# Kernel tuning notes

Measured on AMD Instinct MI355X. Metric: run time of the kernel, lower is better.

Reference implementation:

```python
import jax, jax.numpy as jnp
import numpy as np
import math

B, N, K, H = 2, 2048, 1024, 16
S = K // H  # head dim = 64


def apply_rope(t):
    # t: [b, h, N, s] -> rotary position embedding (rotate-half convention)
    s = t.shape[-1]
    pos = jnp.arange(t.shape[2], dtype=jnp.float32)
    inv_freq = 1.0 / (10000.0 ** (jnp.arange(0, s, 2, dtype=jnp.float32) / s))
    ang = pos[:, None] * inv_freq[None, :]               # [N, s/2]
    cos = jnp.concatenate([jnp.cos(ang), jnp.cos(ang)], axis=-1)  # [N, s]
    sin = jnp.concatenate([jnp.sin(ang), jnp.sin(ang)], axis=-1)
    t1, t2 = t[..., : s // 2], t[..., s // 2:]
    rot = jnp.concatenate([-t2, t1], axis=-1)
    return t * cos + rot * sin


def setup_inputs() -> dict:
    key = jax.random.key(0)
    ks = jax.random.split(key, 6)
    sc = 1.0 / math.sqrt(K)
    x = jax.random.normal(ks[0], (B, N, K), dtype=jnp.float32)
    Wq = jax.random.normal(ks[1], (K, K), dtype=jnp.float32) * sc
    Wk = jax.random.normal(ks[2], (K, K), dtype=jnp.float32) * sc
    Wv = jax.random.normal(ks[3], (K, K), dtype=jnp.float32) * sc
    Wu = jax.random.normal(ks[4], (K, K), dtype=jnp.float32) * sc
    bu = jax.random.normal(ks[5], (K,), dtype=jnp.float32) * 0.01
    mask = jnp.tril(jnp.ones((N, N), dtype=jnp.int32))  # causal
    return {"x": x, "Wq": Wq, "Wk": Wk, "Wv": Wv, "Wu": Wu, "bu": bu, "mask": mask}


def reference(x, Wq, Wk, Wv, Wu, bu, mask):
    b, n, k = x.shape
    h, s = H, S
    # torch Linear: y = x @ W.T
    def proj(W):
        return (x @ W.T).reshape(b, n, h, s).transpose(0, 2, 1, 3)  # [b,h,n,s]
    Q = apply_rope(proj(Wq))
    Kh = apply_rope(proj(Wk))
    V = proj(Wv)
    scores = jnp.einsum('bhqs,bhks->bhqk', Q, Kh) / math.sqrt(s)
    scores = jnp.where(mask[None, None, :, :] == 0, -jnp.inf, scores)
    attn = jax.nn.softmax(scores, axis=-1)
    out = jnp.einsum('bhqk,bhks->bhqs', attn, V)           # [b,h,n,s]
    out = out.transpose(0, 2, 1, 3).reshape(b, n, k)
    return out @ Wu.T + bu
```

## Files before the change

### kernel.cpp

```cpp
#include <hip/hip_runtime.h>
#include <hip/hip_bf16.h>

#define Bq 2
#define Nq 2048
#define Kq 1024
#define Hq 16
#define Sq 64
#define Mq (Bq * Nq)

typedef __attribute__((ext_vector_type(4))) float f32x4;
typedef __attribute__((ext_vector_type(8))) short bf16x8;

__device__ unsigned short g_xb[(size_t)Mq * Kq];
__device__ unsigned short g_Wqb[Kq * Kq];
__device__ unsigned short g_Wkb[Kq * Kq];
__device__ unsigned short g_Wvb[Kq * Kq];
__device__ unsigned short g_Wub[Kq * Kq];
__device__ unsigned short g_Qb[(size_t)Bq * Hq * Nq * Sq];
__device__ unsigned short g_Kb[(size_t)Bq * Hq * Nq * Sq];
__device__ unsigned short g_Vb[(size_t)Bq * Hq * Nq * Sq];
__device__ unsigned short g_Vt[(size_t)Bq * Hq * Sq * Nq];
__device__ unsigned short g_Ao[(size_t)Mq * Kq];

__device__ __forceinline__ unsigned short f2bf(float f) {
    union { float f; unsigned int i; } u; u.f = f;
    unsigned int r = u.i + 0x7FFF + ((u.i >> 16) & 1);
    return (unsigned short)(r >> 16);
}
__device__ __forceinline__ float bf2f(unsigned short u) {
    union { unsigned int i; float f; } v; v.i = ((unsigned int)u) << 16;
    return v.f;
}
__device__ __forceinline__ void async16(const unsigned short* g, unsigned short* l) {
    __builtin_amdgcn_global_load_lds(
        (const __attribute__((address_space(1))) void*)g,
        (__attribute__((address_space(3))) void*)l, 16, 0, 0);
}

__global__ __launch_bounds__(256) void convert_all_kernel(
    const float* __restrict__ x,  const float* __restrict__ wq,
    const float* __restrict__ wk, const float* __restrict__ wv,
    const float* __restrict__ wu)
{
    int i = blockIdx.x * 256 + threadIdx.x;
    const float* src; unsigned short* dst; int off;
    if (i < 1048576) { src = x; dst = g_xb; off = i; }
    else {
        int j = i - 1048576;
        int which = j >> 18;
        off = j & 262143;
        src = (which == 0) ? wq : (which == 1) ? wk : (which == 2) ? wv : wu;
        dst = (which == 0) ? g_Wqb : (which == 1) ? g_Wkb : (which == 2) ? g_Wvb : g_Wub;
    }
    float4 v = ((const float4*)src)[off];
    ushort4 o;
    o.x = f2bf(v.x); o.y = f2bf(v.y); o.z = f2bf(v.z); o.w = f2bf(v.w);
    ((ushort4*)dst)[off] = o;
}

__global__ __launch_bounds__(256) void qkv_gemm_kernel()
{
    __shared__ __align__(16) unsigned short As[128][64];
    __shared__ __align__(16) unsigned short Bs[128][64];

    const int n0 = blockIdx.x * 128;
    const int m0 = blockIdx.y * 128;
    const int which = n0 >> 10;
    const unsigned short* A  = g_xb;
    const unsigned short* Bm = (which == 0) ? g_Wqb : (which == 1) ? g_Wkb : g_Wvb;
    unsigned short* dst      = (which == 0) ? g_Qb : (which == 1) ? g_Kb : g_Vb;
    const int nb = n0 & 1023;

    const int tid = threadIdx.x;
    const int w = tid >> 6, l = tid & 63;
    const int lane16 = l & 15, quad = l >> 4;
    const int wm = (w >> 1) * 64, wn = (w & 1) * 64;

    const int sr = l >> 3;
    const int sc = ((l & 7) ^ sr) * 8;
    const int rsw = (lane16 & 7);

    f32x4 acc[4][4];
#pragma unroll
    for (int mi = 0; mi < 4; ++mi)
#pragma unroll
        for (int ni = 0; ni < 4; ++ni) acc[mi][ni] = (f32x4){0.f, 0.f, 0.f, 0.f};

    for (int kt = 0; kt < Kq; kt += 64) {
        __syncthreads();
#pragma unroll
        for (int c = 0; c < 4; ++c) {
            async16(A  + (size_t)(m0 + 32 * w + 8 * c + sr) * Kq + kt + sc, &As[32 * w + 8 * c][0]);
            async16(Bm + (size_t)(nb + 32 * w + 8 * c + sr) * Kq + kt + sc, &Bs[32 * w + 8 * c][0]);
        }
        __syncthreads();
#pragma unroll
        for (int ks = 0; ks < 2; ++ks) {
            bf16x8 af[4], bfr[4];
#pragma unroll
            for (int mi = 0; mi < 4; ++mi)
                af[mi]  = *(const bf16x8*)&As[wm + mi * 16 + lane16][((ks * 4 + quad) ^ rsw) * 8];
#pragma unroll
            for (int ni = 0; ni < 4; ++ni)
                bfr[ni] = *(const bf16x8*)&Bs[wn + ni * 16 + lane16][((ks * 4 + quad) ^ rsw) * 8];
#pragma unroll
            for (int mi = 0; mi < 4; ++mi)
#pragma unroll
                for (int ni = 0; ni < 4; ++ni)
                    acc[mi][ni] = __builtin_amdgcn_mfma_f32_16x16x32_bf16(af[mi], bfr[ni], acc[mi][ni], 0, 0, 0);
        }
    }

#pragma unroll
    for (int mi = 0; mi < 4; ++mi)
#pragma unroll
        for (int ni = 0; ni < 4; ++ni)
#pragma unroll
            for (int r = 0; r < 4; ++r) {
                int m = m0 + wm + mi * 16 + quad * 4 + r;
                int n = n0 + wn + ni * 16 + lane16;
                unsigned short v = f2bf(acc[mi][ni][r]);
                int b = m >> 11, nn = m & 2047;
                int o = n & 1023, h = o >> 6, s = o & 63;
                dst[(((size_t)b * Hq + h) * Nq + nn) * Sq + s] = v;
            }
}

__global__ __launch_bounds__(256) void rope_kernel()
{
    unsigned short* buf = (blockIdx.y == 0) ? g_Qb : g_Kb;
    const int idx = blockIdx.x * 256 + threadIdx.x;
    const int i  = idx & 31;
    const int n  = (idx >> 5) & (Nq - 1);
    const int bh = idx >> 16;
    const size_t base = ((size_t)bh * Nq + n) * Sq + i;

    float t1 = bf2f(buf[base]);
    float t2 = bf2f(buf[base + 32]);
    float inv_freq = powf(10000.0f, -(float)i / 32.0f);
    float ang = (float)n * inv_freq;
    float sn, cs;
    sincosf(ang, &sn, &cs);
    buf[base]      = f2bf(t1 * cs - t2 * sn);
    buf[base + 32] = f2bf(t2 * cs + t1 * sn);
}

__global__ __launch_bounds__(256) void vtrans_kernel()
{
    __shared__ unsigned short T[64][72];
    const int n0 = blockIdx.x * 64;
    const int bh = blockIdx.y;
    const unsigned short* src = g_Vb + (size_t)bh * Nq * Sq;
    unsigned short* dst       = g_Vt + (size_t)bh * Sq * Nq;
    const int tid = threadIdx.x;
    const int r = tid >> 3, c8 = (tid & 7) * 8;

    uint4 a0 = *(const uint4*)(src + (size_t)(n0 + r) * Sq + c8);
    uint4 a1 = *(const uint4*)(src + (size_t)(n0 + r + 32) * Sq + c8);
    *(uint4*)&T[r][c8] = a0;
    *(uint4*)&T[r + 32][c8] = a1;
    __syncthreads();

    union { ushort4 u4[2]; unsigned short u[8]; } p0, p1;
#pragma unroll
    for (int j = 0; j < 8; ++j) { p0.u[j] = T[c8 + j][r]; p1.u[j] = T[c8 + j][r + 32]; }
    *(uint4*)(dst + (size_t)r * Nq + n0 + c8)        = *(uint4*)&p0;
    *(uint4*)(dst + (size_t)(r + 32) * Nq + n0 + c8) = *(uint4*)&p1;
}

__global__ __launch_bounds__(256) void attn_kernel()
{
    const int bh = blockIdx.x;
    const int qt = 31 - (int)blockIdx.y;
    const int q0 = qt * 64;
    const unsigned short* Qp = g_Qb + (size_t)bh * Nq * Sq;
    const unsigned short* Kp = g_Kb + (size_t)bh * Nq * Sq;
    const unsigned short* Vp = g_Vt + (size_t)bh * Sq * Nq;

    __shared__ __align__(16) unsigned short Ks[2][64][64];
    __shared__ __align__(16) unsigned short Vs[2][64][64];
    __shared__ __align__(16) unsigned short On[16][72];
    __shared__ __align__(16) unsigned short Ps[64][72];

    const int tid = threadIdx.x;
    const int w = tid >> 6, l = tid & 63;
    const int lane16 = l & 15, quad = l >> 4;
    const int sr = l >> 3;
    const int sc = ((l & 7) ^ sr) * 8;
    const int rsw = (lane16 & 7);

    for (int i = tid; i < 16 * 72; i += 256)
        ((unsigned short*)On)[i] = (i < 64) ? 0x3F80 : 0;

    bf16x8 aq0 = *(const bf16x8*)(Qp + (size_t)(q0 + 16 * w + lane16) * Sq + quad * 8);
    bf16x8 aq1 = *(const bf16x8*)(Qp + (size_t)(q0 + 16 * w + lane16) * Sq + quad * 8 + 32);

    f32x4 Oacc[4];
    f32x4 Oext = (f32x4){0.f, 0.f, 0.f, 0.f};
#pragma unroll
    for (int ds = 0; ds < 4; ++ds) Oacc[ds] = (f32x4){0.f, 0.f, 0.f, 0.f};

    const float C1 = 0.18033688f;
    const float C2 = 11.54156036f;

    async16(Kp + (size_t)(16 * w + sr) * Sq + sc,     &Ks[0][16 * w][0]);
    async16(Kp + (size_t)(16 * w + 8 + sr) * Sq + sc, &Ks[0][16 * w + 8][0]);
    async16(Vp + (size_t)(16 * w + sr) * Nq + sc,     &Vs[0][16 * w][0]);
    async16(Vp + (size_t)(16 * w + 8 + sr) * Nq + sc, &Vs[0][16 * w + 8][0]);
    __syncthreads();

    int cur = 0;
    for (int kb = 0; kb <= qt; ++kb) {
        if (kb < qt) {
            int kn = (kb + 1) * 64;
            int nb2 = cur ^ 1;
            async16(Kp + (size_t)(kn + 16 * w + sr) * Sq + sc,     &Ks[nb2][16 * w][0]);
            async16(Kp + (size_t)(kn + 16 * w + 8 + sr) * Sq + sc, &Ks[nb2][16 * w + 8][0]);
            async16(Vp + (size_t)(16 * w + sr) * Nq + kn + sc,     &Vs[nb2][16 * w][0]);
            async16(Vp + (size_t)(16 * w + 8 + sr) * Nq + kn + sc, &Vs[nb2][16 * w + 8][0]);
        }

        f32x4 S[4];
#pragma unroll
        for (int kc = 0; kc < 4; ++kc) S[kc] = (f32x4){0.f, 0.f, 0.f, 0.f};
#pragma unroll
        for (int kc = 0; kc < 4; ++kc) {
            const unsigned short* krow = &Ks[cur][kc * 16 + lane16][0];
            bf16x8 bk0 = *(const bf16x8*)&krow[(quad ^ rsw) * 8];
            bf16x8 bk1 = *(const bf16x8*)&krow[((4 + quad) ^ rsw) * 8];
            S[kc] = __builtin_amdgcn_mfma_f32_16x16x32_bf16(aq0, bk0, S[kc], 0, 0, 0);
            S[kc] = __builtin_amdgcn_mfma_f32_16x16x32_bf16(aq1, bk1, S[kc], 0, 0, 0);
        }

        const int qbase = q0 + 16 * w + quad * 4;
        if (kb == qt) {
#pragma unroll
            for (int kc = 0; kc < 4; ++kc) {
                int kpos = kb * 64 + kc * 16 + lane16;
#pragma unroll
                for (int r = 0; r < 4; ++r)
                    S[kc][r] = (kpos <= qbase + r) ? exp2f(fmaf(S[kc][r], C1, -C2)) : 0.0f;
            }
        } else {
#pragma unroll
            for (int kc = 0; kc < 4; ++kc)
#pragma unroll
                for (int r = 0; r < 4; ++r)
                    S[kc][r] = exp2f(fmaf(S[kc][r], C1, -C2));
        }

#pragma unroll
        for (int kc = 0; kc < 4; ++kc)
#pragma unroll
            for (int r = 0; r < 4; ++r)
                Ps[16 * w + quad * 4 + r][kc * 16 + lane16] =
                    (unsigned short)(__float_as_uint(S[kc][r]) >> 16);

#pragma unroll
        for (int kk = 0; kk < 2; ++kk) {
            bf16x8 pa = *(const bf16x8*)&Ps[16 * w + lane16][kk * 32 + quad * 8];
            bf16x8 be = *(const bf16x8*)&On[lane16][kk * 32 + quad * 8];
#pragma unroll
            for (int ds = 0; ds < 4; ++ds) {
                bf16x8 vb = *(const bf16x8*)&Vs[cur][ds * 16 + lane16][((kk * 4 + quad) ^ rsw) * 8];
                Oacc[ds] = __builtin_amdgcn_mfma_f32_16x16x32_bf16(pa, vb, Oacc[ds], 0, 0, 0);
            }
            Oext = __builtin_amdgcn_mfma_f32_16x16x32_bf16(pa, be, Oext, 0, 0, 0);
        }

        __syncthreads();
        cur ^= 1;
    }

    const int b = bh >> 4, h = bh & 15;
    float inv[4];
#pragma unroll
    for (int r = 0; r < 4; ++r) {
        float lr = __shfl(Oext[r], quad * 16, 64);
        inv[r] = 1.0f / lr;
    }
#pragma unroll
    for (int ds = 0; ds < 4; ++ds)
#pragma unroll
        for (int r = 0; r < 4; ++r) {
            int nn = q0 + 16 * w + quad * 4 + r;
            g_Ao[((size_t)b * Nq + nn) * Kq + h * Sq + ds * 16 + lane16] =
                f2bf(Oacc[ds][r] * inv[r]);
        }
}

__global__ __launch_bounds__(256) void out_gemm_kernel(
    const float* __restrict__ bu, float* __restrict__ out)
{
    __shared__ __align__(16) unsigned short As[128][64];
    __shared__ __align__(16) unsigned short Bs[128][64];

    const int n0 = blockIdx.x * 128;
    const int m0 = blockIdx.y * 128;

    const int tid = threadIdx.x;
    const int w = tid >> 6, l = tid & 63;
    const int lane16 = l & 15, quad = l >> 4;
    const int wm = (w >> 1) * 64, wn = (w & 1) * 64;
    const int sr = l >> 3;
    const int sc = ((l & 7) ^ sr) * 8;
    const int rsw = (lane16 & 7);

    f32x4 acc[4][4];
#pragma unroll
    for (int mi = 0; mi < 4; ++mi)
#pragma unroll
        for (int ni = 0; ni < 4; ++ni) acc[mi][ni] = (f32x4){0.f, 0.f, 0.f, 0.f};

    for (int kt = 0; kt < Kq; kt += 64) {
        __syncthreads();
#pragma unroll
        for (int c = 0; c < 4; ++c) {
            async16(g_Ao  + (size_t)(m0 + 32 * w + 8 * c + sr) * Kq + kt + sc, &As[32 * w + 8 * c][0]);
            async16(g_Wub + (size_t)(n0 + 32 * w + 8 * c + sr) * Kq + kt + sc, &Bs[32 * w + 8 * c][0]);
        }
        __syncthreads();
#pragma unroll
        for (int ks = 0; ks < 2; ++ks) {
            bf16x8 af[4], bfr[4];
#pragma unroll
            for (int mi = 0; mi < 4; ++mi)
                af[mi]  = *(const bf16x8*)&As[wm + mi * 16 + lane16][((ks * 4 + quad) ^ rsw) * 8];
#pragma unroll
            for (int ni = 0; ni < 4; ++ni)
                bfr[ni] = *(const bf16x8*)&Bs[wn + ni * 16 + lane16][((ks * 4 + quad) ^ rsw) * 8];
#pragma unroll
            for (int mi = 0; mi < 4; ++mi)
#pragma unroll
                for (int ni = 0; ni < 4; ++ni)
                    acc[mi][ni] = __builtin_amdgcn_mfma_f32_16x16x32_bf16(af[mi], bfr[ni], acc[mi][ni], 0, 0, 0);
        }
    }

#pragma unroll
    for (int mi = 0; mi < 4; ++mi)
#pragma unroll
        for (int ni = 0; ni < 4; ++ni)
#pragma unroll
            for (int r = 0; r < 4; ++r) {
                int m = m0 + wm + mi * 16 + quad * 4 + r;
                int n = n0 + wn + ni * 16 + lane16;
                out[(size_t)m * Kq + n] = acc[mi][ni][r] + bu[n];
            }
}

extern "C" void kernel_launch(void* const* d_in, const int* in_sizes, int n_in,
                              void* d_out, int out_size, void* d_ws, size_t ws_size,
                              hipStream_t stream)
{
    const float* x  = (const float*)d_in[0];
    const float* Wq = (const float*)d_in[1];
    const float* Wk = (const float*)d_in[2];
    const float* Wv = (const float*)d_in[3];
    const float* Wu = (const float*)d_in[4];
    const float* bu = (const float*)d_in[5];
    float* out = (float*)d_out;

    convert_all_kernel<<<8192, 256, 0, stream>>>(x, Wq, Wk, Wv, Wu);
    qkv_gemm_kernel<<<dim3(24, 32), 256, 0, stream>>>();
    vtrans_kernel<<<dim3(32, 32), 256, 0, stream>>>();
    rope_kernel<<<dim3((Bq * Hq * Nq * 32) / 256, 2), 256, 0, stream>>>();
    attn_kernel<<<dim3(32, 32), 256, 0, stream>>>();
    out_gemm_kernel<<<dim3(8, 32), 256, 0, stream>>>(bu, out);
}
```

Baseline: 228.3 us.

## Double-buffer GEMM LDS tiles, merge rope and V-transpose, use fast trig

Both GEMM kernels now keep two shared-memory buffers and issue the async loads for the next K tile before computing the current one. This replaces two barriers per iteration with one and overlaps global-to-LDS traffic with MFMA work. The rope and V-transpose kernels are merged into one launch, and the rope angle uses exp2f plus __sinf/__cosf instead of powf and sincosf. The costs are double the LDS per block, which may lower occupancy, and lower trig accuracy at large angles, which could matter for positions near 2047. The merged launch also wastes many idle blocks in its V-transpose row, since only 1024 of its 8192 blocks do work.

```diff
diff --git a/kernel.cpp b/kernel.cpp
--- a/kernel.cpp
+++ b/kernel.cpp
@@ -60,8 +60,8 @@
 
 __global__ __launch_bounds__(256) void qkv_gemm_kernel()
 {
-    __shared__ __align__(16) unsigned short As[128][64];
-    __shared__ __align__(16) unsigned short Bs[128][64];
+    __shared__ __align__(16) unsigned short As[2][128][64];
+    __shared__ __align__(16) unsigned short Bs[2][128][64];
 
     const int n0 = blockIdx.x * 128;
     const int m0 = blockIdx.y * 128;
@@ -86,29 +86,40 @@
 #pragma unroll
         for (int ni = 0; ni < 4; ++ni) acc[mi][ni] = (f32x4){0.f, 0.f, 0.f, 0.f};
 
+#pragma unroll
+    for (int c = 0; c < 4; ++c) {
+        async16(A  + (size_t)(m0 + 32 * w + 8 * c + sr) * Kq + sc, &As[0][32 * w + 8 * c][0]);
+        async16(Bm + (size_t)(nb + 32 * w + 8 * c + sr) * Kq + sc, &Bs[0][32 * w + 8 * c][0]);
+    }
+    __syncthreads();
+
+    int cur = 0;
     for (int kt = 0; kt < Kq; kt += 64) {
-        __syncthreads();
-#pragma unroll
-        for (int c = 0; c < 4; ++c) {
-            async16(A  + (size_t)(m0 + 32 * w + 8 * c + sr) * Kq + kt + sc, &As[32 * w + 8 * c][0]);
-            async16(Bm + (size_t)(nb + 32 * w + 8 * c + sr) * Kq + kt + sc, &Bs[32 * w + 8 * c][0]);
-        }
-        __syncthreads();
+        if (kt + 64 < Kq) {
+            int nxt = cur ^ 1;
+#pragma unroll
+            for (int c = 0; c < 4; ++c) {
+                async16(A  + (size_t)(m0 + 32 * w + 8 * c + sr) * Kq + kt + 64 + sc, &As[nxt][32 * w + 8 * c][0]);
+                async16(Bm + (size_t)(nb + 32 * w + 8 * c + sr) * Kq + kt + 64 + sc, &Bs[nxt][32 * w + 8 * c][0]);
+            }
+        }
 #pragma unroll
         for (int ks = 0; ks < 2; ++ks) {
             bf16x8 af[4], bfr[4];
 #pragma unroll
             for (int mi = 0; mi < 4; ++mi)
-                af[mi]  = *(const bf16x8*)&As[wm + mi * 16 + lane16][((ks * 4 + quad) ^ rsw) * 8];
+                af[mi]  = *(const bf16x8*)&As[cur][wm + mi * 16 + lane16][((ks * 4 + quad) ^ rsw) * 8];
 #pragma unroll
             for (int ni = 0; ni < 4; ++ni)
-                bfr[ni] = *(const bf16x8*)&Bs[wn + ni * 16 + lane16][((ks * 4 + quad) ^ rsw) * 8];
+                bfr[ni] = *(const bf16x8*)&Bs[cur][wn + ni * 16 + lane16][((ks * 4 + quad) ^ rsw) * 8];
 #pragma unroll
             for (int mi = 0; mi < 4; ++mi)
 #pragma unroll
                 for (int ni = 0; ni < 4; ++ni)
                     acc[mi][ni] = __builtin_amdgcn_mfma_f32_16x16x32_bf16(af[mi], bfr[ni], acc[mi][ni], 0, 0, 0);
         }
+        __syncthreads();
+        cur ^= 1;
     }
 
 #pragma unroll
@@ -126,46 +137,46 @@
             }
 }
 
-__global__ __launch_bounds__(256) void rope_kernel()
-{
-    unsigned short* buf = (blockIdx.y == 0) ? g_Qb : g_Kb;
-    const int idx = blockIdx.x * 256 + threadIdx.x;
-    const int i  = idx & 31;
-    const int n  = (idx >> 5) & (Nq - 1);
-    const int bh = idx >> 16;
-    const size_t base = ((size_t)bh * Nq + n) * Sq + i;
-
-    float t1 = bf2f(buf[base]);
-    float t2 = bf2f(buf[base + 32]);
-    float inv_freq = powf(10000.0f, -(float)i / 32.0f);
-    float ang = (float)n * inv_freq;
-    float sn, cs;
-    sincosf(ang, &sn, &cs);
-    buf[base]      = f2bf(t1 * cs - t2 * sn);
-    buf[base + 32] = f2bf(t2 * cs + t1 * sn);
-}
-
-__global__ __launch_bounds__(256) void vtrans_kernel()
+__global__ __launch_bounds__(256) void rope_vtrans_kernel()
 {
     __shared__ unsigned short T[64][72];
-    const int n0 = blockIdx.x * 64;
-    const int bh = blockIdx.y;
-    const unsigned short* src = g_Vb + (size_t)bh * Nq * Sq;
-    unsigned short* dst       = g_Vt + (size_t)bh * Sq * Nq;
-    const int tid = threadIdx.x;
-    const int r = tid >> 3, c8 = (tid & 7) * 8;
-
-    uint4 a0 = *(const uint4*)(src + (size_t)(n0 + r) * Sq + c8);
-    uint4 a1 = *(const uint4*)(src + (size_t)(n0 + r + 32) * Sq + c8);
-    *(uint4*)&T[r][c8] = a0;
-    *(uint4*)&T[r + 32][c8] = a1;
-    __syncthreads();
-
-    union { ushort4 u4[2]; unsigned short u[8]; } p0, p1;
-#pragma unroll
-    for (int j = 0; j < 8; ++j) { p0.u[j] = T[c8 + j][r]; p1.u[j] = T[c8 + j][r + 32]; }
-    *(uint4*)(dst + (size_t)r * Nq + n0 + c8)        = *(uint4*)&p0;
-    *(uint4*)(dst + (size_t)(r + 32) * Nq + n0 + c8) = *(uint4*)&p1;
+
+    if (blockIdx.y < 2) {
+        unsigned short* buf = (blockIdx.y == 0) ? g_Qb : g_Kb;
+        const int idx = blockIdx.x * 256 + threadIdx.x;
+        const int i  = idx & 31;
+        const int n  = (idx >> 5) & (Nq - 1);
+        const int bh = idx >> 16;
+        const size_t base = ((size_t)bh * Nq + n) * Sq + i;
+
+        float t1 = bf2f(buf[base]);
+        float t2 = bf2f(buf[base + 32]);
+        float inv_freq = exp2f((float)i * -0.41524101f);
+        float ang = (float)n * inv_freq;
+        float sn = __sinf(ang), cs = __cosf(ang);
+        buf[base]      = f2bf(t1 * cs - t2 * sn);
+        buf[base + 32] = f2bf(t2 * cs + t1 * sn);
+    } else {
+        if (blockIdx.x >= 1024) return;
+        const int n0 = (blockIdx.x & 31) * 64;
+        const int bh = blockIdx.x >> 5;
+        const unsigned short* src = g_Vb + (size_t)bh * Nq * Sq;
+        unsigned short* dst       = g_Vt + (size_t)bh * Sq * Nq;
+        const int tid = threadIdx.x;
+        const int r = tid >> 3, c8 = (tid & 7) * 8;
+
+        uint4 a0 = *(const uint4*)(src + (size_t)(n0 + r) * Sq + c8);
+        uint4 a1 = *(const uint4*)(src + (size_t)(n0 + r + 32) * Sq + c8);
+        *(uint4*)&T[r][c8] = a0;
+        *(uint4*)&T[r + 32][c8] = a1;
+        __syncthreads();
+
+        union { ushort4 u4[2]; unsigned short u[8]; } p0, p1;
+#pragma unroll
+        for (int j = 0; j < 8; ++j) { p0.u[j] = T[c8 + j][r]; p1.u[j] = T[c8 + j][r + 32]; }
+        *(uint4*)(dst + (size_t)r * Nq + n0 + c8)        = *(uint4*)&p0;
+        *(uint4*)(dst + (size_t)(r + 32) * Nq + n0 + c8) = *(uint4*)&p1;
+    }
 }
 
 __global__ __launch_bounds__(256) void attn_kernel()
@@ -292,8 +303,8 @@
 __global__ __launch_bounds__(256) void out_gemm_kernel(
     const float* __restrict__ bu, float* __restrict__ out)
 {
-    __shared__ __align__(16) unsigned short As[128][64];
-    __shared__ __align__(16) unsigned short Bs[128][64];
+    __shared__ __align__(16) unsigned short As[2][128][64];
+    __shared__ __align__(16) unsigned short Bs[2][128][64];
 
     const int n0 = blockIdx.x * 128;
     const int m0 = blockIdx.y * 128;
@@ -312,29 +323,40 @@
 #pragma unroll
         for (int ni = 0; ni < 4; ++ni) acc[mi][ni] = (f32x4){0.f, 0.f, 0.f, 0.f};
 
+#pragma unroll
+    for (int c = 0; c < 4; ++c) {
+        async16(g_Ao  + (size_t)(m0 + 32 * w + 8 * c + sr) * Kq + sc, &As[0][32 * w + 8 * c][0]);
+        async16(g_Wub + (size_t)(n0 + 32 * w + 8 * c + sr) * Kq + sc, &Bs[0][32 * w + 8 * c][0]);
+    }
+    __syncthreads();
+
+    int cur = 0;
     for (int kt = 0; kt < Kq; kt += 64) {
-        __syncthreads();
-#pragma unroll
-        for (int c = 0; c < 4; ++c) {
-            async16(g_Ao  + (size_t)(m0 + 32 * w + 8 * c + sr) * Kq + kt + sc, &As[32 * w + 8 * c][0]);
-            async16(g_Wub + (size_t)(n0 + 32 * w + 8 * c + sr) * Kq + kt + sc, &Bs[32 * w + 8 * c][0]);
-        }
-        __syncthreads();
+        if (kt + 64 < Kq) {
+            int nxt = cur ^ 1;
+#pragma unroll
+            for (int c = 0; c < 4; ++c) {
+                async16(g_Ao  + (size_t)(m0 + 32 * w + 8 * c + sr) * Kq + kt + 64 + sc, &As[nxt][32 * w + 8 * c][0]);
+                async16(g_Wub + (size_t)(n0 + 32 * w + 8 * c + sr) * Kq + kt + 64 + sc, &Bs[nxt][32 * w + 8 * c][0]);
+            }
+        }
 #pragma unroll
         for (int ks = 0; ks < 2; ++ks) {
             bf16x8 af[4], bfr[4];
 #pragma unroll
             for (int mi = 0; mi < 4; ++mi)
-                af[mi]  = *(const bf16x8*)&As[wm + mi * 16 + lane16][((ks * 4 + quad) ^ rsw) * 8];
+                af[mi]  = *(const bf16x8*)&As[cur][wm + mi * 16 + lane16][((ks * 4 + quad) ^ rsw) * 8];
 #pragma unroll
             for (int ni = 0; ni < 4; ++ni)
-                bfr[ni] = *(const bf16x8*)&Bs[wn + ni * 16 + lane16][((ks * 4 + quad) ^ rsw) * 8];
+                bfr[ni] = *(const bf16x8*)&Bs[cur][wn + ni * 16 + lane16][((ks * 4 + quad) ^ rsw) * 8];
 #pragma unroll
             for (int mi = 0; mi < 4; ++mi)
 #pragma unroll
                 for (int ni = 0; ni < 4; ++ni)
                     acc[mi][ni] = __builtin_amdgcn_mfma_f32_16x16x32_bf16(af[mi], bfr[ni], acc[mi][ni], 0, 0, 0);
         }
+        __syncthreads();
+        cur ^= 1;
     }
 
 #pragma unroll
@@ -363,8 +385,7 @@
 
     convert_all_kernel<<<8192, 256, 0, stream>>>(x, Wq, Wk, Wv, Wu);
     qkv_gemm_kernel<<<dim3(24, 32), 256, 0, stream>>>();
-    vtrans_kernel<<<dim3(32, 32), 256, 0, stream>>>();
-    rope_kernel<<<dim3((Bq * Hq * Nq * 32) / 256, 2), 256, 0, stream>>>();
+    rope_vtrans_kernel<<<dim3(8192, 3), 256, 0, stream>>>();
     attn_kernel<<<dim3(32, 32), 256, 0, stream>>>();
     out_gemm_kernel<<<dim3(8, 32), 256, 0, stream>>>(bu, out);
 }
```

Result: faster. 216.8 us (-5.1%).
